# Performance work log

Hardware: AMD Instinct MI355X
Metric: run time of the kernel (lower is better)

## Reference

```python
import jax, jax.numpy as jnp
import numpy as np
import math

IMG_W, IMG_H = 800, 320
N_POINTS = 72
N_STRIPS = 71
S = 36   # sample_points
P = 192  # n_priors
C = 64   # prior_fea_channels == fc_hidden_dim
B = 32

SAMPLE_X_IDX = (np.linspace(0, 1, S) * N_STRIPS).astype(np.int64)
PRIOR_FEAT_YS = np.flip(1.0 - SAMPLE_X_IDX.astype(np.float32) / N_STRIPS).copy()
PRIOR_YS = np.linspace(1, 0, N_POINTS, dtype=np.float32)


def _init_priors():
    emb = np.zeros((P, 3), np.float32)
    left = P // 8
    bottom = P * 3 // 4
    strip = 0.5 / (left // 2 - 1)
    bstrip = 1.0 / (bottom // 4 + 1)
    for i in range(left):
        emb[i] = ((i // 2) * strip, 0.0, 0.16 if i % 2 == 0 else 0.32)
    for i in range(left, left + bottom):
        emb[i] = (0.0, ((i - left) // 4 + 1) * bstrip, 0.2 * (i % 4 + 1))
    for i in range(left + bottom, P):
        emb[i] = (((i - left - bottom) // 2) * strip, 1.0, 0.68 if i % 2 == 0 else 0.84)
    pri = np.zeros((P, 6 + N_POINTS), np.float32)
    pri[:, 2:5] = emb
    pri[:, 6:] = (emb[:, 1:2] * (IMG_W - 1)
                  + (1 - PRIOR_YS[None] - emb[:, 0:1]) * IMG_H / np.tan(emb[:, 2:3] * math.pi + 1e-5)) / (IMG_W - 1)
    return pri.astype(np.float32), pri[:, 6 + SAMPLE_X_IDX].astype(np.float32)


def _bn(x, p):
    # p: (4, C) = gamma, beta, running_mean, running_var; channel axis = 1 (eval mode)
    g, b, m, v = p[0], p[1], p[2], p[3]
    shape = [1] * x.ndim
    shape[1] = -1
    return (x - m.reshape(shape)) * (g.reshape(shape) / jnp.sqrt(v.reshape(shape) + 1e-5)) + b.reshape(shape)


def _conv1d(x, w, pad):
    # x (N, Cin, L), w (Cout, Cin, K); the torch module uses (9,1) conv on (...,36,1)
    return jax.lax.conv_general_dilated(x, w, (1,), [(pad, pad)],
                                        dimension_numbers=('NCH', 'OIH', 'NCH'))


def _grid_sample(img, gx, gy):
    # F.grid_sample: bilinear, align_corners=True, padding_mode='zeros'
    # img (B,C,H,W); gx, gy (B,P,S) in [-1,1] -> out (B,C,P,S)
    b, c, h, w = img.shape
    x = (gx + 1.0) * 0.5 * (w - 1)
    y = (gy + 1.0) * 0.5 * (h - 1)
    x0 = jnp.floor(x)
    y0 = jnp.floor(y)
    imgf = img.reshape(b, c, h * w)

    def gather(xi, yi):
        valid = (xi >= 0) & (xi <= w - 1) & (yi >= 0) & (yi <= h - 1)
        xi_c = jnp.clip(xi, 0, w - 1).astype(jnp.int32)
        yi_c = jnp.clip(yi, 0, h - 1).astype(jnp.int32)
        idx = yi_c * w + xi_c
        v = jax.vmap(lambda f, ix: f[:, ix])(imgf, idx)  # (B,C,P,S)
        return v * valid[:, None].astype(img.dtype)

    wx = x - x0
    wy = y - y0
    return (gather(x0, y0) * ((1 - wx) * (1 - wy))[:, None]
            + gather(x0 + 1, y0) * (wx * (1 - wy))[:, None]
            + gather(x0, y0 + 1) * ((1 - wx) * wy)[:, None]
            + gather(x0 + 1, y0 + 1) * (wx * wy)[:, None])


def _resize_nearest(x, oh, ow):
    # torch F.interpolate default: nearest, idx = floor(i * in / out)
    b, c, h, w = x.shape
    ri = (jnp.arange(oh) * h) // oh
    rj = (jnp.arange(ow) * w) // ow
    return x[:, :, ri][:, :, :, rj]


def _forward(x0, x1, x2, priors0, priors_feat0, conv_w, bn_conv, cat_w0, cat_w1, cat_w2,
             bn_cat, fkey_w, bn_key, fval_w, fval_b, fq_w, fq_b, attnW_w, attnW_b,
             fc_w, fc_b, ln_g, ln_b, mlp_w, mlp_b, reg_w, reg_b, cls_w, cls_b):
    feats = [x2, x1, x0]  # batch_features = x[-3:] reversed -> coarsest first
    b = x0.shape[0]
    prior_ys = jnp.asarray(PRIOR_YS)
    feat_ys = jnp.asarray(PRIOR_FEAT_YS)
    sx_idx = jnp.asarray(SAMPLE_X_IDX)
    priors = jnp.broadcast_to(priors0, (b, P, 6 + N_POINTS))
    priors_feat = jnp.broadcast_to(priors_feat0, (b, P, S))
    cat_ws = [cat_w0, cat_w1, cat_w2]
    stage_rois = []
    preds = []
    for stage in range(3):
        fmap = feats[stage]
        prior_xs = priors_feat[:, :, ::-1]  # torch.flip(dim=2)
        gx = prior_xs * 2.0 - 1.0
        gy = jnp.broadcast_to((feat_ys * 2.0 - 1.0)[None, None, :], (b, P, S))
        pooled = _grid_sample(fmap, gx, gy)                 # (B,C,P,S)
        pooled = pooled.transpose(0, 2, 1, 3).reshape(b * P, C, S)
        stage_rois.append(pooled)
        # ROIGather.roi_fea: per-stage (9,1) conv + BN + ReLU, then cat conv
        trans = [jax.nn.relu(_bn(_conv1d(stage_rois[i], conv_w[i], 4), bn_conv[i]))
                 for i in range(stage + 1)]
        cat = jnp.concatenate(trans, axis=1)
        cat = jax.nn.relu(_bn(_conv1d(cat, cat_ws[stage], 4), bn_cat[stage]))  # (B*P,C,S)
        # fc + LayerNorm + ReLU
        roi = cat.reshape(b * P, C * S) @ fc_w + fc_b
        mu = roi.mean(-1, keepdims=True)
        var = roi.var(-1, keepdims=True)
        roi = (roi - mu) / jnp.sqrt(var + 1e-5) * ln_g + ln_b
        roi = jax.nn.relu(roi).reshape(b, P, C)
        # attention: grouped-conv1d query (per-prior scalar), key/value on resized map
        query = jax.nn.relu(roi * fq_w[None, :, None] + fq_b[None, :, None])
        key = jax.nn.relu(_bn(jnp.einsum('bchw,oc->bohw', fmap, fkey_w), bn_key))
        key = _resize_nearest(key, 10, 25).reshape(b, C, 250)
        value = jnp.einsum('bchw,oc->bohw', fmap, fval_w) + fval_b[None, :, None, None]
        value = _resize_nearest(value, 10, 25).reshape(b, C, 250)
        sim = jax.nn.softmax(jnp.einsum('bpc,bck->bpk', query, key) * (C ** -0.5), axis=-1)
        context = jnp.einsum('bpk,bck->bpc', sim, value)
        context = context * attnW_w[None, :, None] + attnW_b[None, :, None]
        roi = roi + context  # dropout inactive in eval
        # heads (source bug: reg and cls share the SAME Linear applied twice)
        f = roi.reshape(b * P, C)
        h = jax.nn.relu(f @ mlp_w + mlp_b)
        h = jax.nn.relu(h @ mlp_w + mlp_b)
        cls_logits = (h @ cls_w + cls_b).reshape(b, P, 2)
        reg = (h @ reg_w + reg_b).reshape(b, P, 4 + N_POINTS)
        p2 = priors[..., 2] + reg[..., 0]
        p3 = priors[..., 3] + reg[..., 1]
        p4 = priors[..., 4] + reg[..., 2]
        p5 = reg[..., 3]
        geom = (p3[..., None] * (IMG_W - 1)
                + (1.0 - prior_ys[None, None, :] - p2[..., None]) * IMG_H
                / jnp.tan(p4[..., None] * math.pi + 1e-5)) / (IMG_W - 1)
        head = jnp.stack([cls_logits[..., 0], cls_logits[..., 1], p2, p3, p4, p5], axis=-1)
        pred = jnp.concatenate([head, geom + reg[..., 4:]], axis=-1)
        preds.append(pred)
        if stage != 2:
            lines = jax.lax.stop_gradient(jnp.concatenate([head, geom], axis=-1))
            priors = lines
            priors_feat = lines[..., 6 + sx_idx]
    return jnp.stack(preds, axis=0)  # (3, B, P, 78)


def setup_inputs() -> dict:
    key = jax.random.key(0)
    ks = list(jax.random.split(key, 24))
    f32 = jnp.float32
    rn = lambda k, sh, s: jax.random.normal(k, sh, dtype=f32) * s

    def bn_p(k, *lead):
        k1, k2, k3, k4 = jax.random.split(k, 4)
        g = 0.75 + 0.5 * jax.random.uniform(k1, lead + (C,), dtype=f32)
        b = 0.1 * jax.random.normal(k2, lead + (C,), dtype=f32)
        m = 0.1 * jax.random.normal(k3, lead + (C,), dtype=f32)
        v = 0.75 + 0.5 * jax.random.uniform(k4, lead + (C,), dtype=f32)
        return jnp.stack([g, b, m, v], axis=-2)  # (..., 4, C)

    pri, prif = _init_priors()
    return {
        'x0': rn(ks[0], (B, C, IMG_H // 8, IMG_W // 8), 1.0),
        'x1': rn(ks[1], (B, C, IMG_H // 16, IMG_W // 16), 1.0),
        'x2': rn(ks[2], (B, C, IMG_H // 32, IMG_W // 32), 1.0),
        'priors0': jnp.asarray(pri),
        'priors_feat0': jnp.asarray(prif),
        'conv_w': rn(ks[3], (3, C, C, 9), 0.04),
        'bn_conv': bn_p(ks[4], 3),
        'cat_w0': rn(ks[5], (C, C, 9), 0.04),
        'cat_w1': rn(ks[6], (C, 2 * C, 9), 0.03),
        'cat_w2': rn(ks[7], (C, 3 * C, 9), 0.025),
        'bn_cat': bn_p(ks[8], 3),
        'fkey_w': rn(ks[9], (C, C), 0.12),
        'bn_key': bn_p(ks[10]),
        'fval_w': rn(ks[11], (C, C), 0.12),
        'fval_b': rn(ks[12], (C,), 0.05),
        'fq_w': 1.0 + rn(ks[13], (P,), 0.1),
        'fq_b': rn(ks[14], (P,), 0.05),
        'attnW_w': rn(ks[15], (P,), 0.02),
        'attnW_b': rn(ks[16], (P,), 0.02),
        'fc_w': rn(ks[17], (C * S, C), 0.02),
        'fc_b': rn(ks[18], (C,), 0.02),
        'ln_g': jnp.ones((C,), f32),
        'ln_b': jnp.zeros((C,), f32),
        'mlp_w': rn(ks[19], (C, C), 0.12),
        'mlp_b': rn(ks[20], (C,), 0.02),
        'reg_w': rn(ks[21], (C, 4 + N_POINTS), 0.001),
        'reg_b': rn(ks[22], (4 + N_POINTS,), 0.001),
        'cls_w': rn(ks[23], (C, 2), 0.001),
        'cls_b': jnp.zeros((2,), f32),
    }


def reference(x0, x1, x2, priors0, priors_feat0, conv_w, bn_conv, cat_w0, cat_w1, cat_w2,
              bn_cat, fkey_w, bn_key, fval_w, fval_b, fq_w, fq_b, attnW_w, attnW_b,
              fc_w, fc_b, ln_g, ln_b, mlp_w, mlp_b, reg_w, reg_b, cls_w, cls_b):
    return _forward(x0, x1, x2, priors0, priors_feat0, conv_w, bn_conv, cat_w0, cat_w1,
                    cat_w2, bn_cat, fkey_w, bn_key, fval_w, fval_b, fq_w, fq_b,
                    attnW_w, attnW_b, fc_w, fc_b, ln_g, ln_b, mlp_w, mlp_b,
                    reg_w, reg_b, cls_w, cls_b)
```

## Files before the change

kernel.cpp:

```cpp
#include <hip/hip_runtime.h>
#include <hip/hip_bf16.h>
#include <math.h>

typedef __hip_bfloat16 bf16;
typedef __attribute__((ext_vector_type(8))) short short8v;
typedef __attribute__((ext_vector_type(4))) float float4v;

static constexpr int kB = 32;
static constexpr int kP = 192;
static constexpr int kS = 36;
static constexpr int kC = 64;
static constexpr int kRows = kB * kP;
static constexpr float kPI = 3.14159265358979323846f;

__device__ __constant__ int d_SX[36] = {
  0,2,4,6,8,10,12,14,16,18,20,22,24,26,28,30,32,34,
  36,38,40,42,44,46,48,50,52,54,56,58,60,62,64,66,68,71};

__device__ __forceinline__ float b2f(bf16 v) { return __bfloat162float(v); }
__device__ __forceinline__ unsigned short f2bu(float f) {
  bf16 h = __float2bfloat16(f);
  return *reinterpret_cast<unsigned short*>(&h);
}
__device__ __forceinline__ float su2f(unsigned short u) {
  bf16 t; *reinterpret_cast<unsigned short*>(&t) = u; return __bfloat162float(t);
}
#define MFMA16 __builtin_amdgcn_mfma_f32_16x16x32_bf16

__global__ __launch_bounds__(256) void k_wprep(
    const float* __restrict__ src, bf16* __restrict__ dst, int CI, int total)
{
  int d = blockIdx.x * 256 + threadIdx.x;
  if (d >= total) return;
  int j   = d & 7;
  int l   = (d >> 3) & 63;
  int wid = (d >> 9) & 3;
  int r   = d >> 11;
  int nchi = CI >> 5;
  int chi = r % nchi, t = r / nchi;
  int co = wid * 16 + (l & 15);
  int ci = chi * 32 + 8 * (l >> 4) + j;
  dst[d] = __float2bfloat16(src[(co * CI + ci) * 9 + t]);
}

__global__ __launch_bounds__(256) void k_wprep_fc(
    const float* __restrict__ src, bf16* __restrict__ dst)
{
  int d = blockIdx.x * 256 + threadIdx.x;
  if (d >= 2304 * 64) return;
  int j    = d & 7;
  int l    = (d >> 3) & 63;
  int tile = (d >> 9) & 3;
  int kk   = d >> 11;
  int cout = tile * 16 + (l & 15);
  int k    = kk * 32 + 8 * (l >> 4) + j;
  int c = k & 63, s = k >> 6;
  dst[d] = __float2bfloat16(src[(c * kS + s) * kC + cout]);
}

__global__ __launch_bounds__(256) void k_wprep_mlpT(
    const float* __restrict__ src, bf16* __restrict__ dst)
{
  int d = blockIdx.x * 256 + threadIdx.x;
  if (d >= 64 * 64) return;
  int co = d >> 6, ci = d & 63;
  dst[d] = __float2bfloat16(src[ci * 64 + co]);
}

__global__ __launch_bounds__(256) void k_wprep_rct(
    const float* __restrict__ regw, const float* __restrict__ clsw,
    const float* __restrict__ regb, const float* __restrict__ clsb,
    bf16* __restrict__ dst, float* __restrict__ rcb)
{
  int d = blockIdx.x * 256 + threadIdx.x;
  if (d < 80 * 64) {
    int o = d >> 6, ci = d & 63;
    float v = (o < 76) ? regw[ci * 76 + o] : (o < 78 ? clsw[ci * 2 + (o - 76)] : 0.f);
    dst[d] = __float2bfloat16(v);
  }
  if (d < 80) rcb[d] = (d < 76) ? regb[d] : (d < 78 ? clsb[d - 76] : 0.f);
}

__global__ __launch_bounds__(256) void k_transpose(
    const float* __restrict__ src, bf16* __restrict__ dst, int h, int w)
{
  __shared__ float tile[64][65];
  const int by = blockIdx.x;
  const int b = by / h, y = by % h;
  const int lane = threadIdx.x & 63, wq = threadIdx.x >> 6;
  for (int x0 = 0; x0 < w; x0 += 64) {
    #pragma unroll
    for (int cc = 0; cc < 16; ++cc) {
      int c = wq * 16 + cc;
      int x = x0 + lane;
      if (x < w) tile[c][lane] = src[((size_t)(b*kC + c)*h + y)*w + x];
    }
    __syncthreads();
    #pragma unroll
    for (int xx = 0; xx < 16; ++xx) {
      int x = x0 + wq * 16 + xx;
      if (x < w) dst[((size_t)(b*h + y)*w + x)*kC + lane] = __float2bfloat16(tile[lane][wq*16 + xx]);
    }
    __syncthreads();
  }
}

__global__ __launch_bounds__(256) void k_trans(
    const bf16* __restrict__ fmapT, int h, int w,
    const float* __restrict__ pfeat0, const float* __restrict__ pfeatw, int stage,
    const bf16* __restrict__ wfrag,
    const float* __restrict__ bnp,
    bf16* __restrict__ transOut)
{
  __shared__ __align__(16) bf16 poolT[2][56][64];
  __shared__ float bsc[kC], bsh[kC];
  const int tid = threadIdx.x;
  const int row0 = blockIdx.x * 2, b = row0 / kP;

  if (tid < kC) {
    float g = bnp[tid], bb = bnp[kC + tid];
    float m = bnp[2*kC + tid], v = bnp[3*kC + tid];
    float sc = g / sqrtf(v + 1e-5f);
    bsc[tid] = sc; bsh[tid] = bb - m * sc;
  }
  unsigned int* pz = (unsigned int*)&poolT[0][0][0];
  for (int e = tid; e < 2*56*32; e += 256) pz[e] = 0u;
  __syncthreads();

  const int lc = tid & 7;
  for (int idx = tid >> 3; idx < 2*kS; idx += 32) {
    int r2 = idx / kS, s = idx % kS;
    int row = row0 + r2, p = row % kP;
    float px = (stage == 0) ? pfeat0[p*kS + (kS-1-s)] : pfeatw[row*kS + (kS-1-s)];
    float fy = 1.0f - (float)d_SX[kS-1-s] / 71.0f;
    float x = px * (float)(w - 1);
    float y = fy * (float)(h - 1);
    float x0f = floorf(x), y0f = floorf(y);
    float wx = x - x0f, wy = y - y0f;
    int xi = (int)x0f, yi = (int)y0f;
    float a8[8];
    #pragma unroll
    for (int j = 0; j < 8; ++j) a8[j] = 0.f;
    #pragma unroll
    for (int cy = 0; cy < 2; ++cy) {
      #pragma unroll
      for (int cx = 0; cx < 2; ++cx) {
        int xx = xi + cx, yy = yi + cy;
        if (xx >= 0 && xx < w && yy >= 0 && yy < h) {
          float wgt = (cx ? wx : 1.f - wx) * (cy ? wy : 1.f - wy);
          short8v v = *(const short8v*)&fmapT[((size_t)(b*h + yy)*w + xx)*kC + lc*8];
          #pragma unroll
          for (int j = 0; j < 8; ++j)
            a8[j] += su2f((unsigned short)v[j]) * wgt;
        }
      }
    }
    uint4 pk;
    pk.x = (unsigned)f2bu(a8[0]) | ((unsigned)f2bu(a8[1]) << 16);
    pk.y = (unsigned)f2bu(a8[2]) | ((unsigned)f2bu(a8[3]) << 16);
    pk.z = (unsigned)f2bu(a8[4]) | ((unsigned)f2bu(a8[5]) << 16);
    pk.w = (unsigned)f2bu(a8[6]) | ((unsigned)f2bu(a8[7]) << 16);
    int lr = s + 4;
    *reinterpret_cast<uint4*>(&poolT[r2][lr][((lc + lr) & 7)*8]) = pk;
  }
  __syncthreads();

  const int wv = tid >> 6, lane = tid & 63;
  const int r2 = wv & 1, cp = wv >> 1;
  const int lm = lane & 15, lq = lane >> 4;
  float4v acc[2][3] = {{{0,0,0,0},{0,0,0,0},{0,0,0,0}},{{0,0,0,0},{0,0,0,0},{0,0,0,0}}};
  #pragma unroll
  for (int t = 0; t < 9; ++t) {
    #pragma unroll
    for (int chi = 0; chi < 2; ++chi) {
      short8v a0 = *(const short8v*)&wfrag[(((t*2 + chi)*4 + cp*2 + 0)*64 + lane)*8];
      short8v a1 = *(const short8v*)&wfrag[(((t*2 + chi)*4 + cp*2 + 1)*64 + lane)*8];
      #pragma unroll
      for (int nt = 0; nt < 3; ++nt) {
        int rr = nt*16 + lm + t;
        int sl = chi*4 + lq;
        short8v bb = *(const short8v*)&poolT[r2][rr][((sl + rr) & 7)*8];
        acc[0][nt] = MFMA16(a0, bb, acc[0][nt], 0, 0, 0);
        acc[1][nt] = MFMA16(a1, bb, acc[1][nt], 0, 0, 0);
      }
    }
  }
  #pragma unroll
  for (int c2 = 0; c2 < 2; ++c2) {
    const int c4 = (cp*2 + c2)*16 + 4*lq;
    float s0 = bsc[c4], s1 = bsc[c4+1], s2 = bsc[c4+2], s3 = bsc[c4+3];
    float h0 = bsh[c4], h1 = bsh[c4+1], h2 = bsh[c4+2], h3 = bsh[c4+3];
    #pragma unroll
    for (int nt = 0; nt < 3; ++nt) {
      int s = nt*16 + lm;
      if (s < kS) {
        uint2 pk;
        pk.x = (unsigned)f2bu(fmaxf(acc[c2][nt][0]*s0 + h0, 0.f))
             | ((unsigned)f2bu(fmaxf(acc[c2][nt][1]*s1 + h1, 0.f)) << 16);
        pk.y = (unsigned)f2bu(fmaxf(acc[c2][nt][2]*s2 + h2, 0.f))
             | ((unsigned)f2bu(fmaxf(acc[c2][nt][3]*s3 + h3, 0.f)) << 16);
        *reinterpret_cast<uint2*>(&transOut[((size_t)(row0+r2)*kS + s)*kC + c4]) = pk;
      }
    }
  }
}

template<int NCI>
__global__ __launch_bounds__(256) void k_catconv(
    const bf16* __restrict__ t0, const bf16* __restrict__ t1, const bf16* __restrict__ t2,
    const bf16* __restrict__ wfrag,
    const float* __restrict__ bnp, bf16* __restrict__ catOut)
{
  constexpr int CB = NCI/8;
  __shared__ __align__(16) bf16 poolT[2][56][NCI];
  __shared__ float bsc[kC], bsh[kC];
  const int tid = threadIdx.x;
  const int row0 = blockIdx.x * 2;
  if (tid < kC) {
    float g = bnp[tid], bb = bnp[kC + tid];
    float m = bnp[2*kC + tid], v = bnp[3*kC + tid];
    float sc = g / sqrtf(v + 1e-5f);
    bsc[tid] = sc; bsh[tid] = bb - m * sc;
  }
  unsigned int* pz = (unsigned int*)&poolT[0][0][0];
  for (int e = tid; e < 2*56*NCI/2; e += 256) pz[e] = 0u;
  __syncthreads();

  const bf16* tb[3] = {t0, t1, t2};
  for (int cc = tid; cc < 2*kS*CB; cc += 256) {
    int r2 = cc / (kS*CB), rem = cc % (kS*CB);
    int s = rem / CB, cb = rem % CB;
    int ch = cb * 8, i = ch >> 6, c = ch & 63;
    const short8v* src = (const short8v*)&tb[i][((size_t)(row0+r2)*kS + s)*kC + c];
    int lr = s + 4;
    int sl = (cb & ~7) | ((cb + lr) & 7);
    *(short8v*)&poolT[r2][lr][sl*8] = *src;
  }
  __syncthreads();

  const int wv = tid >> 6, lane = tid & 63;
  const int r2 = wv & 1, cp = wv >> 1;
  const int lm = lane & 15, lq = lane >> 4;
  float4v acc[2][3] = {{{0,0,0,0},{0,0,0,0},{0,0,0,0}},{{0,0,0,0},{0,0,0,0},{0,0,0,0}}};
  #pragma unroll
  for (int t = 0; t < 9; ++t) {
    #pragma unroll
    for (int chi = 0; chi < NCI/32; ++chi) {
      short8v a0 = *(const short8v*)&wfrag[(((t*(NCI/32) + chi)*4 + cp*2 + 0)*64 + lane)*8];
      short8v a1 = *(const short8v*)&wfrag[(((t*(NCI/32) + chi)*4 + cp*2 + 1)*64 + lane)*8];
      #pragma unroll
      for (int nt = 0; nt < 3; ++nt) {
        int rr = nt*16 + lm + t;
        int sl0 = chi*4 + lq;
        int sl = (sl0 & ~7) | ((sl0 + rr) & 7);
        short8v bb = *(const short8v*)&poolT[r2][rr][sl*8];
        acc[0][nt] = MFMA16(a0, bb, acc[0][nt], 0, 0, 0);
        acc[1][nt] = MFMA16(a1, bb, acc[1][nt], 0, 0, 0);
      }
    }
  }
  #pragma unroll
  for (int c2 = 0; c2 < 2; ++c2) {
    const int c4 = (cp*2 + c2)*16 + 4*lq;
    float s0 = bsc[c4], s1 = bsc[c4+1], s2 = bsc[c4+2], s3 = bsc[c4+3];
    float h0 = bsh[c4], h1 = bsh[c4+1], h2 = bsh[c4+2], h3 = bsh[c4+3];
    #pragma unroll
    for (int nt = 0; nt < 3; ++nt) {
      int s = nt*16 + lm;
      if (s < kS) {
        uint2 pk;
        pk.x = (unsigned)f2bu(fmaxf(acc[c2][nt][0]*s0 + h0, 0.f))
             | ((unsigned)f2bu(fmaxf(acc[c2][nt][1]*s1 + h1, 0.f)) << 16);
        pk.y = (unsigned)f2bu(fmaxf(acc[c2][nt][2]*s2 + h2, 0.f))
             | ((unsigned)f2bu(fmaxf(acc[c2][nt][3]*s3 + h3, 0.f)) << 16);
        *reinterpret_cast<uint2*>(&catOut[((size_t)(row0+r2)*kS + s)*kC + c4]) = pk;
      }
    }
  }
}

__global__ __launch_bounds__(64) void k_keyval(
    const float* __restrict__ fmap, int h, int w,
    const float* __restrict__ fkeyw, const float* __restrict__ bnk,
    const float* __restrict__ fvalw, const float* __restrict__ fvalb,
    bf16* __restrict__ key_pc, bf16* __restrict__ val_ck)
{
  const int tid = threadIdx.x;
  const int blk = blockIdx.x, b = blk >> 8, pos = blk & 255;
  if (pos >= 250) {
    key_pc[((size_t)b*256 + pos)*kC + tid] = __float2bfloat16(0.f);
    val_ck[((size_t)b*kC + tid)*256 + pos] = __float2bfloat16(0.f);
    return;
  }
  const int i = pos / 25, j = pos % 25;
  const int yi = (i * h) / 10, xj = (j * w) / 25;
  __shared__ float fv[kC];
  fv[tid] = fmap[((size_t)(b*kC + tid) * h + yi) * w + xj];
  __syncthreads();
  float ka = 0.f, va = 0.f;
  const float* kr = fkeyw + tid * kC;
  const float* vr = fvalw + tid * kC;
  for (int c = 0; c < kC; ++c) { float f = fv[c]; ka += f * kr[c]; va += f * vr[c]; }
  float g = bnk[tid], bb = bnk[kC + tid];
  float m = bnk[2*kC + tid], v = bnk[3*kC + tid];
  float sc = g / sqrtf(v + 1e-5f), sh = bb - m * sc;
  key_pc[((size_t)b*256 + pos)*kC + tid] = __float2bfloat16(fmaxf(ka*sc + sh, 0.f));
  val_ck[((size_t)b*kC + tid)*256 + pos] = __float2bfloat16(va + fvalb[tid]);
}

__global__ __launch_bounds__(256) void k_tail(
    const bf16* __restrict__ catOut, const bf16* __restrict__ wfc,
    const float* __restrict__ fcb, const float* __restrict__ lng, const float* __restrict__ lnb,
    const bf16* __restrict__ key_pc, const bf16* __restrict__ val_ck,
    const float* __restrict__ fqw, const float* __restrict__ fqb,
    const float* __restrict__ aww, const float* __restrict__ awb,
    const bf16* __restrict__ mlpwT, const float* __restrict__ mlpb,
    const bf16* __restrict__ rcT, const float* __restrict__ rcb,
    const float* __restrict__ priors0, const float* __restrict__ priw_in, int stage,
    float* __restrict__ out, float* __restrict__ priw_out, float* __restrict__ pfeat_out)
{
  __shared__ __align__(16) float partS[4][16][68];
  __shared__ __align__(16) float roiL[12][68];
  __shared__ __align__(16) bf16 q[16][72];
  __shared__ __align__(16) bf16 P[16][264];
  __shared__ float rsum[16];
  __shared__ __align__(16) bf16 r2b[16][72];
  __shared__ __align__(16) bf16 h1l[16][72];
  __shared__ __align__(16) bf16 h2l[16][72];
  __shared__ float regc[12][84];
  __shared__ float ev[12][8];

  const int tid = threadIdx.x;
  const int blk = blockIdx.x, b = blk >> 4, tile = blk & 15;
  const int p0 = tile * 12;
  const int lane = tid & 63, wq = tid >> 6;
  const int lm = lane & 15, lq = lane >> 4;
  float (*S)[264] = (float (*)[264])&partS[0][0][0];

  { unsigned* z1 = (unsigned*)&q[0][0];
    for (int e = tid; e < 16*72/2; e += 256) z1[e] = 0u;
    unsigned* z2 = (unsigned*)&r2b[0][0];
    for (int e = tid; e < 16*72/2; e += 256) z2[e] = 0u; }

  {
    float4v fa[4] = {{0,0,0,0},{0,0,0,0},{0,0,0,0},{0,0,0,0}};
    int r0c = p0 + lm; if (r0c > p0 + 11) r0c = p0 + 11;
    const bf16* bb0 = catOut + (size_t)(b*kP + r0c) * 2304 + lq * 8;
    for (int kk = wq * 18; kk < wq * 18 + 18; ++kk) {
      short8v bf0 = *(const short8v*)&bb0[kk * 32];
      #pragma unroll
      for (int t = 0; t < 4; ++t) {
        short8v afrag = *(const short8v*)&wfc[((kk*4 + t)*64 + lane)*8];
        fa[t] = MFMA16(afrag, bf0, fa[t], 0, 0, 0);
      }
    }
    #pragma unroll
    for (int t = 0; t < 4; ++t)
      *(float4v*)&partS[wq][lm][t*16 + lq*4] = fa[t];
  }
  __syncthreads();
  for (int r = wq; r < 12; r += 4) {
    float v = partS[0][r][lane] + partS[1][r][lane] + partS[2][r][lane] + partS[3][r][lane]
            + fcb[lane];
    float s1 = v, s2 = v * v;
    #pragma unroll
    for (int m = 32; m; m >>= 1) { s1 += __shfl_xor(s1, m, 64); s2 += __shfl_xor(s2, m, 64); }
    float mu = s1 * (1.f/64.f);
    float var = s2 * (1.f/64.f) - mu * mu;
    float y = fmaxf((v - mu) * rsqrtf(var + 1e-5f) * lng[lane] + lnb[lane], 0.f);
    roiL[r][lane] = y;
    int p = p0 + r;
    q[r][lane] = __float2bfloat16(fmaxf(y * fqw[p] + fqb[p], 0.f));
  }
  __syncthreads();

  {
    float4v acc[4] = {{0,0,0,0},{0,0,0,0},{0,0,0,0},{0,0,0,0}};
    #pragma unroll
    for (int ks = 0; ks < 2; ++ks) {
      short8v aq0 = *(const short8v*)&q[lm][ks*32 + 8*lq];
      #pragma unroll
      for (int nt = 0; nt < 4; ++nt) {
        int pos = (wq*4 + nt)*16 + lm;
        short8v bk = *(const short8v*)&key_pc[((size_t)(b*256 + pos))*kC + ks*32 + 8*lq];
        acc[nt] = MFMA16(aq0, bk, acc[nt], 0, 0, 0);
      }
    }
    #pragma unroll
    for (int nt = 0; nt < 4; ++nt)
      #pragma unroll
      for (int r = 0; r < 4; ++r)
        S[lq*4 + r][(wq*4 + nt)*16 + lm] = acc[nt][r] * 0.125f;
  }
  __syncthreads();

  {
    int r = tid >> 4, g = tid & 15;
    float mx = -1e30f;
    #pragma unroll 16
    for (int k = 0; k < 16; ++k) { int c = g + 16*k; if (c < 250) mx = fmaxf(mx, S[r][c]); }
    #pragma unroll
    for (int m = 1; m < 16; m <<= 1) mx = fmaxf(mx, __shfl_xor(mx, m, 64));
    float sum = 0.f;
    #pragma unroll 16
    for (int k = 0; k < 16; ++k) {
      int c = g + 16*k;
      float e = 0.f;
      if (c < 250) { e = expf(S[r][c] - mx); sum += e; }
      P[r][c] = __float2bfloat16(e);
    }
    #pragma unroll
    for (int m = 1; m < 16; m <<= 1) sum += __shfl_xor(sum, m, 64);
    if (g == 0) rsum[r] = sum;
  }
  __syncthreads();

  {
    float4v acc = {0,0,0,0};
    #pragma unroll
    for (int ks = 0; ks < 8; ++ks) {
      short8v bv = *(const short8v*)&val_ck[((size_t)(b*kC + wq*16 + lm))*256 + ks*32 + 8*lq];
      short8v ap0 = *(const short8v*)&P[lm][ks*32 + 8*lq];
      acc = MFMA16(ap0, bv, acc, 0, 0, 0);
    }
    #pragma unroll
    for (int r = 0; r < 4; ++r) {
      int pl = lq*4 + r;
      if (pl < 12) {
        int p = p0 + pl, c = wq*16 + lm;
        float ctx = acc[r] / rsum[pl];
        r2b[pl][c] = __float2bfloat16(roiL[pl][c] + ctx * aww[p] + awb[p]);
      }
    }
  }
  __syncthreads();

  {
    float4v acc = {0,0,0,0};
    #pragma unroll
    for (int ks = 0; ks < 2; ++ks) {
      short8v a0 = *(const short8v*)&r2b[lm][ks*32 + 8*lq];
      short8v bw = *(const short8v*)&mlpwT[(wq*16 + lm)*kC + ks*32 + 8*lq];
      acc = MFMA16(a0, bw, acc, 0, 0, 0);
    }
    #pragma unroll
    for (int r = 0; r < 4; ++r) {
      int rw = lq*4 + r, col = wq*16 + lm;
      h1l[rw][col] = __float2bfloat16(fmaxf(acc[r] + mlpb[col], 0.f));
    }
  }
  __syncthreads();
  {
    float4v acc = {0,0,0,0};
    #pragma unroll
    for (int ks = 0; ks < 2; ++ks) {
      short8v a0 = *(const short8v*)&h1l[lm][ks*32 + 8*lq];
      short8v bw = *(const short8v*)&mlpwT[(wq*16 + lm)*kC + ks*32 + 8*lq];
      acc = MFMA16(a0, bw, acc, 0, 0, 0);
    }
    #pragma unroll
    for (int r = 0; r < 4; ++r) {
      int rw = lq*4 + r, col = wq*16 + lm;
      h2l[rw][col] = __float2bfloat16(fmaxf(acc[r] + mlpb[col], 0.f));
    }
  }
  __syncthreads();
  for (int ntile = wq; ntile < 5; ntile += 4) {
    float4v acc = {0,0,0,0};
    #pragma unroll
    for (int ks = 0; ks < 2; ++ks) {
      short8v a0 = *(const short8v*)&h2l[lm][ks*32 + 8*lq];
      short8v bw = *(const short8v*)&rcT[(ntile*16 + lm)*kC + ks*32 + 8*lq];
      acc = MFMA16(a0, bw, acc, 0, 0, 0);
    }
    #pragma unroll
    for (int r = 0; r < 4; ++r) {
      int rw = lq*4 + r, col = ntile*16 + lm;
      if (rw < 12) regc[rw][col] = acc[r] + rcb[col];
    }
  }
  __syncthreads();

  if (tid < 12) {
    int r = tid, p = p0 + r, grow = b*kP + p;
    float pr2, pr3, pr4;
    if (stage == 0) {
      pr2 = priors0[p*78 + 2]; pr3 = priors0[p*78 + 3]; pr4 = priors0[p*78 + 4];
    } else {
      const float* pw = priw_in + (size_t)grow * 78;
      pr2 = pw[2]; pr3 = pw[3]; pr4 = pw[4];
    }
    float p2 = pr2 + regc[r][0], p3 = pr3 + regc[r][1];
    float p4 = pr4 + regc[r][2], p5 = regc[r][3];
    ev[r][0] = p2; ev[r][1] = p3; ev[r][2] = p4; ev[r][3] = p5;
    ev[r][4] = 320.f / tanf(p4 * kPI + 1e-5f);
    ev[r][5] = regc[r][76]; ev[r][6] = regc[r][77];
  }
  __syncthreads();
  for (int e = tid; e < 12*78; e += 256) {
    int r = e / 78, o = e % 78;
    int p = p0 + r, grow = b*kP + p;
    float p2 = ev[r][0], p3 = ev[r][1], t320 = ev[r][4];
    float g = 0.f, v;
    if (o >= 6) g = (p3 * 799.f + ((float)(o-6) / 71.f - p2) * t320) / 799.f;
    if      (o == 0) v = ev[r][5];
    else if (o == 1) v = ev[r][6];
    else if (o == 2) v = p2;
    else if (o == 3) v = p3;
    else if (o == 4) v = ev[r][2];
    else if (o == 5) v = ev[r][3];
    else             v = g + regc[r][4 + (o - 6)];
    out[((size_t)(stage*kB + b)*kP + p) * 78 + o] = v;
    if (stage < 2) priw_out[(size_t)grow*78 + o] = (o < 6) ? v : g;
  }
  if (stage < 2) {
    for (int e = tid; e < 12*kS; e += 256) {
      int r = e / kS, si = e % kS;
      int grow = b*kP + p0 + r;
      float p2 = ev[r][0], p3 = ev[r][1], t320 = ev[r][4];
      pfeat_out[(size_t)grow*kS + si] =
          (p3 * 799.f + ((float)d_SX[si] / 71.f - p2) * t320) / 799.f;
    }
  }
}

extern "C" void kernel_launch(void* const* d_in, const int* in_sizes, int n_in,
                              void* d_out, int out_size, void* d_ws, size_t ws_size,
                              hipStream_t stream) {
  const float* x0      = (const float*)d_in[0];
  const float* x1      = (const float*)d_in[1];
  const float* x2      = (const float*)d_in[2];
  const float* priors0 = (const float*)d_in[3];
  const float* pfeat0  = (const float*)d_in[4];
  const float* conv_w  = (const float*)d_in[5];
  const float* bn_conv = (const float*)d_in[6];
  const float* cat_w[3]= {(const float*)d_in[7], (const float*)d_in[8], (const float*)d_in[9]};
  const float* bn_cat  = (const float*)d_in[10];
  const float* fkey_w  = (const float*)d_in[11];
  const float* bn_key  = (const float*)d_in[12];
  const float* fval_w  = (const float*)d_in[13];
  const float* fval_b  = (const float*)d_in[14];
  const float* fq_w    = (const float*)d_in[15];
  const float* fq_b    = (const float*)d_in[16];
  const float* attnW_w = (const float*)d_in[17];
  const float* attnW_b = (const float*)d_in[18];
  const float* fc_w    = (const float*)d_in[19];
  const float* fc_b    = (const float*)d_in[20];
  const float* ln_g    = (const float*)d_in[21];
  const float* ln_b    = (const float*)d_in[22];
  const float* mlp_w   = (const float*)d_in[23];
  const float* mlp_b   = (const float*)d_in[24];
  const float* reg_w   = (const float*)d_in[25];
  const float* reg_b   = (const float*)d_in[26];
  const float* cls_w   = (const float*)d_in[27];
  const float* cls_b   = (const float*)d_in[28];
  float* out = (float*)d_out;

  char* ws = (char*)d_ws;
  size_t off = 0;
  auto alloc = [&](size_t bytes) { void* pp = ws + off; off += (bytes + 255) & ~(size_t)255; return pp; };
  bf16* trans[3];
  for (int i = 0; i < 3; ++i) trans[i] = (bf16*)alloc((size_t)kRows * 2304 * sizeof(bf16));
  bf16*  catout = (bf16*) alloc((size_t)kRows * 2304 * sizeof(bf16));
  bf16*  key_pc[3]; bf16* val_ck[3];
  for (int i = 0; i < 3; ++i) {
    key_pc[i] = (bf16*)alloc((size_t)kB * 256 * kC * sizeof(bf16));
    val_ck[i] = (bf16*)alloc((size_t)kB * kC * 256 * sizeof(bf16));
  }
  float* priwA  = (float*)alloc((size_t)kRows * 78 * sizeof(float));
  float* priwB  = (float*)alloc((size_t)kRows * 78 * sizeof(float));
  float* pfw    = (float*)alloc((size_t)kRows * kS * sizeof(float));
  bf16* wtr[3], *wcat[3];
  const int catCI[3] = {64, 128, 192};
  for (int i = 0; i < 3; ++i) wtr[i]  = (bf16*)alloc((size_t)64*64*9 * sizeof(bf16));
  for (int i = 0; i < 3; ++i) wcat[i] = (bf16*)alloc((size_t)64*catCI[i]*9 * sizeof(bf16));
  bf16* wfc    = (bf16*)alloc((size_t)2304*64 * sizeof(bf16));
  bf16* mlpwT  = (bf16*)alloc((size_t)64*64 * sizeof(bf16));
  bf16* rcT    = (bf16*)alloc((size_t)80*64 * sizeof(bf16));
  float* rcb   = (float*)alloc((size_t)80 * sizeof(float));
  const int hd[3] = {10, 20, 40}, wd[3] = {25, 50, 100};
  bf16* fmapT[3];
  for (int i = 0; i < 3; ++i)
    fmapT[i] = (bf16*)alloc((size_t)kB * hd[i] * wd[i] * kC * sizeof(bf16));
  (void)ws_size; (void)in_sizes; (void)n_in; (void)out_size;

  for (int i = 0; i < 3; ++i) {
    int tot = 64*64*9;
    k_wprep<<<(tot+255)/256, 256, 0, stream>>>(conv_w + i*64*64*9, wtr[i], 64, tot);
  }
  for (int i = 0; i < 3; ++i) {
    int tot = 64*catCI[i]*9;
    k_wprep<<<(tot+255)/256, 256, 0, stream>>>(cat_w[i], wcat[i], catCI[i], tot);
  }
  k_wprep_fc<<<(2304*64+255)/256, 256, 0, stream>>>(fc_w, wfc);
  k_wprep_mlpT<<<16, 256, 0, stream>>>(mlp_w, mlpwT);
  k_wprep_rct<<<20, 256, 0, stream>>>(reg_w, cls_w, reg_b, cls_b, rcT, rcb);
  const float* fmaps[3] = {x2, x1, x0};
  for (int i = 0; i < 3; ++i) {
    k_transpose<<<kB*hd[i], 256, 0, stream>>>(fmaps[i], fmapT[i], hd[i], wd[i]);
    k_keyval<<<kB*256, 64, 0, stream>>>(fmaps[i], hd[i], wd[i], fkey_w, bn_key,
                                        fval_w, fval_b, key_pc[i], val_ck[i]);
  }

  for (int st = 0; st < 3; ++st) {
    const int h = hd[st], w = wd[st];
    const float* priw_in  = (st == 1) ? priwA : priwB;
    float*       priw_out = (st == 0) ? priwA : priwB;
    k_trans<<<kRows/2, 256, 0, stream>>>(fmapT[st], h, w, pfeat0, pfw, st,
                                         wtr[st], bn_conv + st*4*kC, trans[st]);
    if (st == 0)
      k_catconv<64><<<kRows/2, 256, 0, stream>>>(trans[0], trans[1], trans[2], wcat[0],
                                                 bn_cat + st*4*kC, catout);
    else if (st == 1)
      k_catconv<128><<<kRows/2, 256, 0, stream>>>(trans[0], trans[1], trans[2], wcat[1],
                                                  bn_cat + st*4*kC, catout);
    else
      k_catconv<192><<<kRows/2, 256, 0, stream>>>(trans[0], trans[1], trans[2], wcat[2],
                                                  bn_cat + st*4*kC, catout);
    k_tail<<<kB*16, 256, 0, stream>>>(catout, wfc, fc_b, ln_g, ln_b,
                                      key_pc[st], val_ck[st], fq_w, fq_b, attnW_w, attnW_b,
                                      mlpwT, mlp_b, rcT, rcb,
                                      priors0, priw_in, st, out, priw_out, pfw);
  }
}
```

Before: 487.1 us.

## Rewrite cat conv with 32x32 MFMA tiles over 8 rows per block

Replaces the concat-conv kernel's 16x16x32 MFMA path with 32x32x16 MFMA tiles. Each block now covers 8 prior rows (288 spatial positions) using 3 waves, and input channels are staged into LDS in 64-channel chunks, one per source tensor. Weights are re-laid out for the 32-wide fragment format. The aim is more reuse of each weight fragment across positions and fewer blocks. The cost is more accumulator registers and extra barriers between chunks.

```diff
diff --git a/kernel.cpp b/kernel.cpp
--- a/kernel.cpp
+++ b/kernel.cpp
@@ -5,6 +5,7 @@
 typedef __hip_bfloat16 bf16;
 typedef __attribute__((ext_vector_type(8))) short short8v;
 typedef __attribute__((ext_vector_type(4))) float float4v;
+typedef __attribute__((ext_vector_type(16))) float float16v;
 
 static constexpr int kB = 32;
 static constexpr int kP = 192;
@@ -26,6 +27,7 @@
   bf16 t; *reinterpret_cast<unsigned short*>(&t) = u; return __bfloat162float(t);
 }
 #define MFMA16 __builtin_amdgcn_mfma_f32_16x16x32_bf16
+#define MFMA32 __builtin_amdgcn_mfma_f32_32x32x16_bf16
 
 __global__ __launch_bounds__(256) void k_wprep(
     const float* __restrict__ src, bf16* __restrict__ dst, int CI, int total)
@@ -40,6 +42,22 @@
   int chi = r % nchi, t = r / nchi;
   int co = wid * 16 + (l & 15);
   int ci = chi * 32 + 8 * (l >> 4) + j;
+  dst[d] = __float2bfloat16(src[(co * CI + ci) * 9 + t]);
+}
+
+__global__ __launch_bounds__(256) void k_wprep32(
+    const float* __restrict__ src, bf16* __restrict__ dst, int CI, int total)
+{
+  int d = blockIdx.x * 256 + threadIdx.x;
+  if (d >= total) return;
+  int j  = d & 7;
+  int l  = (d >> 3) & 63;
+  int ct = (d >> 9) & 1;
+  int r  = d >> 10;
+  int nchi = CI >> 4;
+  int chi = r % nchi, t = r / nchi;
+  int co = ct * 32 + (l & 31);
+  int ci = chi * 16 + 8 * (l >> 5) + j;
   dst[d] = __float2bfloat16(src[(co * CI + ci) * 9 + t]);
 }
 
@@ -205,75 +223,93 @@
   }
 }
 
-template<int NCI>
-__global__ __launch_bounds__(256) void k_catconv(
+template<int NCHUNK>
+__global__ __launch_bounds__(192) void k_catconv32(
     const bf16* __restrict__ t0, const bf16* __restrict__ t1, const bf16* __restrict__ t2,
     const bf16* __restrict__ wfrag,
     const float* __restrict__ bnp, bf16* __restrict__ catOut)
 {
-  constexpr int CB = NCI/8;
-  __shared__ __align__(16) bf16 poolT[2][56][NCI];
+  constexpr int NCHI16 = NCHUNK * 4;
+  __shared__ __align__(16) bf16 chunk[352][64];
   __shared__ float bsc[kC], bsh[kC];
   const int tid = threadIdx.x;
-  const int row0 = blockIdx.x * 2;
+  const int row0 = blockIdx.x * 8;
   if (tid < kC) {
     float g = bnp[tid], bb = bnp[kC + tid];
     float m = bnp[2*kC + tid], v = bnp[3*kC + tid];
     float sc = g / sqrtf(v + 1e-5f);
     bsc[tid] = sc; bsh[tid] = bb - m * sc;
   }
-  unsigned int* pz = (unsigned int*)&poolT[0][0][0];
-  for (int e = tid; e < 2*56*NCI/2; e += 256) pz[e] = 0u;
-  __syncthreads();
-
   const bf16* tb[3] = {t0, t1, t2};
-  for (int cc = tid; cc < 2*kS*CB; cc += 256) {
-    int r2 = cc / (kS*CB), rem = cc % (kS*CB);
-    int s = rem / CB, cb = rem % CB;
-    int ch = cb * 8, i = ch >> 6, c = ch & 63;
-    const short8v* src = (const short8v*)&tb[i][((size_t)(row0+r2)*kS + s)*kC + c];
-    int lr = s + 4;
-    int sl = (cb & ~7) | ((cb + lr) & 7);
-    *(short8v*)&poolT[r2][lr][sl*8] = *src;
-  }
-  __syncthreads();
-
-  const int wv = tid >> 6, lane = tid & 63;
-  const int r2 = wv & 1, cp = wv >> 1;
-  const int lm = lane & 15, lq = lane >> 4;
-  float4v acc[2][3] = {{{0,0,0,0},{0,0,0,0},{0,0,0,0}},{{0,0,0,0},{0,0,0,0},{0,0,0,0}}};
+
+  const int wv = tid / 64, lane = tid & 63;
+  const int l5 = lane >> 5, l31 = lane & 31;
+  int baseR[3], rA[3], sA[3];
   #pragma unroll
-  for (int t = 0; t < 9; ++t) {
-    #pragma unroll
-    for (int chi = 0; chi < NCI/32; ++chi) {
-      short8v a0 = *(const short8v*)&wfrag[(((t*(NCI/32) + chi)*4 + cp*2 + 0)*64 + lane)*8];
-      short8v a1 = *(const short8v*)&wfrag[(((t*(NCI/32) + chi)*4 + cp*2 + 1)*64 + lane)*8];
-      #pragma unroll
-      for (int nt = 0; nt < 3; ++nt) {
-        int rr = nt*16 + lm + t;
-        int sl0 = chi*4 + lq;
-        int sl = (sl0 & ~7) | ((sl0 + rr) & 7);
-        short8v bb = *(const short8v*)&poolT[r2][rr][sl*8];
-        acc[0][nt] = MFMA16(a0, bb, acc[0][nt], 0, 0, 0);
-        acc[1][nt] = MFMA16(a1, bb, acc[1][nt], 0, 0, 0);
-      }
-    }
-  }
+  for (int i = 0; i < 3; ++i) {
+    int m = (3*wv + i)*32 + l31;
+    rA[i] = m / kS; sA[i] = m % kS;
+    baseR[i] = rA[i]*44 + sA[i];
+  }
+  float16v acc[3][2];
   #pragma unroll
-  for (int c2 = 0; c2 < 2; ++c2) {
-    const int c4 = (cp*2 + c2)*16 + 4*lq;
-    float s0 = bsc[c4], s1 = bsc[c4+1], s2 = bsc[c4+2], s3 = bsc[c4+3];
-    float h0 = bsh[c4], h1 = bsh[c4+1], h2 = bsh[c4+2], h3 = bsh[c4+3];
-    #pragma unroll
-    for (int nt = 0; nt < 3; ++nt) {
-      int s = nt*16 + lm;
-      if (s < kS) {
+  for (int i = 0; i < 3; ++i)
+    #pragma unroll
+    for (int ct = 0; ct < 2; ++ct)
+      #pragma unroll
+      for (int r = 0; r < 16; ++r) acc[i][ct][r] = 0.f;
+
+  #pragma unroll
+  for (int kc = 0; kc < NCHUNK; ++kc) {
+    if (kc > 0) __syncthreads();
+    for (int e = tid; e < 352*8; e += 192) {
+      int lr = e >> 3, slot = e & 7;
+      int rr = lr / 44, sp = lr % 44;
+      short8v v = {0,0,0,0,0,0,0,0};
+      if (sp >= 4 && sp < 40)
+        v = *(const short8v*)&tb[kc][((size_t)(row0 + rr)*kS + (sp - 4))*kC + slot*8];
+      *(short8v*)&chunk[lr][((slot + lr) & 7)*8] = v;
+    }
+    __syncthreads();
+    #pragma unroll
+    for (int t = 0; t < 9; ++t) {
+      #pragma unroll
+      for (int ks = 0; ks < 4; ++ks) {
+        int slot = ks*2 + l5;
+        short8v bfrag[3];
+        #pragma unroll
+        for (int i = 0; i < 3; ++i) {
+          int rr = baseR[i] + t;
+          bfrag[i] = *(const short8v*)&chunk[rr][((slot + rr) & 7)*8];
+        }
+        int chig = kc*4 + ks;
+        #pragma unroll
+        for (int ct = 0; ct < 2; ++ct) {
+          short8v a = *(const short8v*)&wfrag[(((t*NCHI16 + chig)*2 + ct)*64 + lane)*8];
+          acc[0][ct] = MFMA32(a, bfrag[0], acc[0][ct], 0, 0, 0);
+          acc[1][ct] = MFMA32(a, bfrag[1], acc[1][ct], 0, 0, 0);
+          acc[2][ct] = MFMA32(a, bfrag[2], acc[2][ct], 0, 0, 0);
+        }
+      }
+    }
+  }
+
+  #pragma unroll
+  for (int i = 0; i < 3; ++i) {
+    bf16* ob = catOut + ((size_t)(row0 + rA[i])*kS + sA[i])*kC;
+    #pragma unroll
+    for (int ct = 0; ct < 2; ++ct) {
+      #pragma unroll
+      for (int g = 0; g < 4; ++g) {
+        int cb = ct*32 + 8*g + 4*l5;
+        float s0 = bsc[cb], s1 = bsc[cb+1], s2 = bsc[cb+2], s3 = bsc[cb+3];
+        float h0 = bsh[cb], h1 = bsh[cb+1], h2 = bsh[cb+2], h3 = bsh[cb+3];
         uint2 pk;
-        pk.x = (unsigned)f2bu(fmaxf(acc[c2][nt][0]*s0 + h0, 0.f))
-             | ((unsigned)f2bu(fmaxf(acc[c2][nt][1]*s1 + h1, 0.f)) << 16);
-        pk.y = (unsigned)f2bu(fmaxf(acc[c2][nt][2]*s2 + h2, 0.f))
-             | ((unsigned)f2bu(fmaxf(acc[c2][nt][3]*s3 + h3, 0.f)) << 16);
-        *reinterpret_cast<uint2*>(&catOut[((size_t)(row0+r2)*kS + s)*kC + c4]) = pk;
+        pk.x = (unsigned)f2bu(fmaxf(acc[i][ct][4*g+0]*s0 + h0, 0.f))
+             | ((unsigned)f2bu(fmaxf(acc[i][ct][4*g+1]*s1 + h1, 0.f)) << 16);
+        pk.y = (unsigned)f2bu(fmaxf(acc[i][ct][4*g+2]*s2 + h2, 0.f))
+             | ((unsigned)f2bu(fmaxf(acc[i][ct][4*g+3]*s3 + h3, 0.f)) << 16);
+        *reinterpret_cast<uint2*>(&ob[cb]) = pk;
       }
     }
   }
@@ -590,7 +626,7 @@
   }
   for (int i = 0; i < 3; ++i) {
     int tot = 64*catCI[i]*9;
-    k_wprep<<<(tot+255)/256, 256, 0, stream>>>(cat_w[i], wcat[i], catCI[i], tot);
+    k_wprep32<<<(tot+255)/256, 256, 0, stream>>>(cat_w[i], wcat[i], catCI[i], tot);
   }
   k_wprep_fc<<<(2304*64+255)/256, 256, 0, stream>>>(fc_w, wfc);
   k_wprep_mlpT<<<16, 256, 0, stream>>>(mlp_w, mlpwT);
@@ -609,13 +645,13 @@
     k_trans<<<kRows/2, 256, 0, stream>>>(fmapT[st], h, w, pfeat0, pfw, st,
                                          wtr[st], bn_conv + st*4*kC, trans[st]);
     if (st == 0)
-      k_catconv<64><<<kRows/2, 256, 0, stream>>>(trans[0], trans[1], trans[2], wcat[0],
-                                                 bn_cat + st*4*kC, catout);
+      k_catconv32<1><<<kRows/8, 192, 0, stream>>>(trans[0], trans[1], trans[2], wcat[0],
+                                                  bn_cat + st*4*kC, catout);
     else if (st == 1)
-      k_catconv<128><<<kRows/2, 256, 0, stream>>>(trans[0], trans[1], trans[2], wcat[1],
+      k_catconv32<2><<<kRows/8, 192, 0, stream>>>(trans[0], trans[1], trans[2], wcat[1],
                                                   bn_cat + st*4*kC, catout);
     else
-      k_catconv<192><<<kRows/2, 256, 0, stream>>>(trans[0], trans[1], trans[2], wcat[2],
+      k_catconv32<3><<<kRows/8, 192, 0, stream>>>(trans[0], trans[1], trans[2], wcat[2],
                                                   bn_cat + st*4*kC, catout);
     k_tail<<<kB*16, 256, 0, stream>>>(catout, wfc, fc_b, ln_g, ln_b,
                                       key_pc[st], val_ck[st], fq_w, fq_b, attnW_w, attnW_b,
```

After: 622.0 us. 1.28x slower.
